# Optimization experiments

Measured on AMD Instinct MI355X. Metric: run time of the kernel, lower is better.

The kernel has to match this reference:

```python
import jax, jax.numpy as jnp
import numpy as np

B, L, H, D, M = 4, 2048, 16, 64, 128
EPS = 1e-6


def _create_projection_matrix(key, m, d):
    nb_full_blocks = m // d
    keys = jax.random.split(key, nb_full_blocks + 2)
    blocks = []
    for i in range(nb_full_blocks):
        unstructured = jax.random.normal(keys[i], (d, d), dtype=jnp.float32)
        q, _ = jnp.linalg.qr(unstructured)
        blocks.append(q.T)
    remaining = m - nb_full_blocks * d
    if remaining > 0:
        unstructured = jax.random.normal(keys[nb_full_blocks], (d, d), dtype=jnp.float32)
        q, _ = jnp.linalg.qr(unstructured)
        blocks.append(q.T[:remaining])
    final = jnp.concatenate(blocks, axis=0)  # [m, d]
    multiplier = jnp.linalg.norm(jax.random.normal(keys[-1], (m, d), dtype=jnp.float32), axis=1)
    return multiplier[:, None] * final


def setup_inputs() -> dict:
    key = jax.random.key(0)
    kq, kk, kv, kp = jax.random.split(key, 4)
    return {
        "q": jax.random.normal(kq, (B, L, H, D), dtype=jnp.float32),
        "k": jax.random.normal(kk, (B, L, H, D), dtype=jnp.float32),
        "v": jax.random.normal(kv, (B, L, H, D), dtype=jnp.float32),
        "projection_matrix": _create_projection_matrix(kp, M, D),
    }


def _softmax_kernel(data, proj, is_query, eps=EPS):
    # data: [B,L,H,D], proj: [M,D]
    data = (data.shape[-1] ** -0.25) * data
    ratio = proj.shape[0] ** -0.5
    data_dash = jnp.einsum('blhd,md->blhm', data, proj)  # [B,L,H,M]
    diag = jnp.sum(data * data, axis=-1, keepdims=True) * 0.5  # [B,L,H,1]
    if is_query:
        mx = jnp.max(data_dash, axis=-1, keepdims=True)
    else:
        mx = jnp.max(data_dash, axis=(1, 3), keepdims=True)
    return ratio * (jnp.exp(data_dash - diag - mx) + eps)


def reference(q, k, v, projection_matrix):
    qp = _softmax_kernel(q, projection_matrix, True)   # [B,L,H,M]
    kp = _softmax_kernel(k, projection_matrix, False)  # [B,L,H,M]
    # move L to the front for the causal scan
    qs = jnp.swapaxes(qp, 0, 1)  # [L,B,H,M]
    ks = jnp.swapaxes(kp, 0, 1)  # [L,B,H,M]
    vs = jnp.swapaxes(v, 0, 1)   # [L,B,H,D]

    def step(carry, inp):
        s, dsum = carry                 # s: [B,H,M,D], dsum: [B,H,M]
        q_t, k_t, v_t = inp
        s = s + k_t[..., :, None] * v_t[..., None, :]  # outer product accumulate
        dsum = dsum + k_t
        num = jnp.einsum('bhmd,bhm->bhd', s, q_t)      # [B,H,D]
        den = jnp.einsum('bhm,bhm->bh', q_t, dsum)     # [B,H]
        return (s, dsum), (num, den)

    init = (jnp.zeros((qs.shape[1], qs.shape[2], qs.shape[3], vs.shape[3]), qs.dtype),
            jnp.zeros_like(ks[0]))
    _, (nums, dens) = jax.lax.scan(step, init, (qs, ks, vs))
    av = jnp.swapaxes(nums, 0, 1)          # [B,L,H,D]
    norm = jnp.swapaxes(dens, 0, 1)[..., None]  # [B,L,H,1]
    return av / norm
```

## Files before the change

### kernel.cpp

```cpp
#include <hip/hip_runtime.h>
#include <math.h>

#define B_ 4
#define L_ 2048
#define H_ 16
#define D_ 64
#define M_ 128
#define TC_ 64
#define NC_ (L_ / TC_)
#define EPSK 1e-6f
#define DATA_SCALE 0.35355339059327379f
#define RATIO 0.08838834764831845f

typedef __bf16 bf16;
typedef bf16 bf16x4 __attribute__((ext_vector_type(4)));
typedef bf16 bf16x8 __attribute__((ext_vector_type(8)));
typedef float floatx4 __attribute__((ext_vector_type(4)));

#define PK64 72
#define FS_ 136

__device__ __forceinline__ unsigned pk(bf16 a, bf16 b) {
    return (unsigned)__builtin_bit_cast(unsigned short, a) |
           ((unsigned)__builtin_bit_cast(unsigned short, b) << 16);
}

__device__ __forceinline__ unsigned enc_f(float f) {
    unsigned u = __float_as_uint(f);
    return (u & 0x80000000u) ? ~u : (u | 0x80000000u);
}
__device__ __forceinline__ float dec_f(unsigned u) {
    unsigned b = (u & 0x80000000u) ? (u ^ 0x80000000u) : ~u;
    return __uint_as_float(b);
}

__global__ __launch_bounds__(256) void proj_split(const float* __restrict__ proj,
                                                  bf16* __restrict__ pfh,
                                                  bf16* __restrict__ pfl,
                                                  unsigned* __restrict__ mx) {
    int f = blockIdx.x * 256 + threadIdx.x;
    if (blockIdx.x == 0 && threadIdx.x < B_ * H_) mx[threadIdx.x] = 0u;
    int tc = f >> 7, k0h = (f >> 6) & 1, lane = f & 63;
    int lr = lane & 15, quad = lane >> 4;
    const float* src = proj + (16 * tc + lr) * 64 + k0h * 32 + quad * 8;
    float4 x0 = *(const float4*)src;
    float4 x1 = *(const float4*)(src + 4);
    float a[8] = {x0.x, x0.y, x0.z, x0.w, x1.x, x1.y, x1.z, x1.w};
    bf16x8 hi, lo;
#pragma unroll
    for (int e = 0; e < 8; e++) {
        bf16 h = (bf16)a[e];
        hi[e] = h;
        lo[e] = (bf16)(a[e] - (float)h);
    }
    *(bf16x8*)(pfh + (size_t)f * 8) = hi;
    *(bf16x8*)(pfl + (size_t)f * 8) = lo;
}

__global__ __launch_bounds__(256) void feat_max(const float* __restrict__ k,
                                                const bf16* __restrict__ pfh,
                                                unsigned* __restrict__ mxk) {
    __shared__ float wred[4];
    int tid = threadIdx.x;
    int blk = blockIdx.x;
    int c = blk & 31, h = (blk >> 5) & 15, b = blk >> 9;
    int l0 = c * 64;
    int w = tid >> 6, lane = tid & 63, lr = lane & 15, quad = lane >> 4;

    const float* drow = k +
        ((size_t)(b * L_ + l0 + 16 * w + lr) * H_ + h) * D_ + quad * 8;
    bf16x8 ah[2];
#pragma unroll
    for (int k0 = 0; k0 < 2; k0++) {
        float4 x0 = *(const float4*)(drow + k0 * 32);
        float4 x1 = *(const float4*)(drow + k0 * 32 + 4);
        float a[8] = {x0.x, x0.y, x0.z, x0.w, x1.x, x1.y, x1.z, x1.w};
#pragma unroll
        for (int e = 0; e < 8; e++) ah[k0][e] = (bf16)(DATA_SCALE * a[e]);
    }

    floatx4 acc[8];
#pragma unroll
    for (int tc = 0; tc < 8; tc++) acc[tc] = (floatx4){0.f, 0.f, 0.f, 0.f};
    const bf16x8* ph = (const bf16x8*)pfh + lane;
#pragma unroll
    for (int tc = 0; tc < 8; tc++)
#pragma unroll
        for (int k0 = 0; k0 < 2; k0++) {
            bf16x8 bh = ph[(tc * 2 + k0) * 64];
            acc[tc] = __builtin_amdgcn_mfma_f32_16x16x32_bf16(ah[k0], bh, acc[tc], 0, 0, 0);
        }

    float mm = acc[0][0];
#pragma unroll
    for (int tc = 0; tc < 8; tc++)
#pragma unroll
        for (int reg = 0; reg < 4; reg++) mm = fmaxf(mm, acc[tc][reg]);
#pragma unroll
    for (int off = 1; off < 64; off <<= 1) mm = fmaxf(mm, __shfl_xor(mm, off, 64));
    if (lane == 0) wred[w] = mm;
    __syncthreads();
    if (tid == 0) {
        float g = fmaxf(fmaxf(wred[0], wred[1]), fmaxf(wred[2], wred[3]));
        atomicMax(&mxk[b * H_ + h], enc_f(g));
    }
}

__global__ __launch_bounds__(256) void feat_k(const float* __restrict__ kin,
                                              const bf16* __restrict__ pfh,
                                              const bf16* __restrict__ pfl,
                                              const unsigned* __restrict__ mxk,
                                              bf16* __restrict__ kp) {
    __shared__ __align__(16) bf16 sc[64 * 130];
    int tid = threadIdx.x;
    int blk = blockIdx.x;
    int c = blk & 31, h = (blk >> 5) & 15, b = blk >> 9;
    int l0 = c * 64;
    int w = tid >> 6, lane = tid & 63, lr = lane & 15, quad = lane >> 4;

    const float* drow = kin +
        ((size_t)(b * L_ + l0 + 16 * w + lr) * H_ + h) * D_ + quad * 8;
    bf16x8 ah[2], al[2];
    float ss = 0.f;
#pragma unroll
    for (int k0 = 0; k0 < 2; k0++) {
        float4 x0 = *(const float4*)(drow + k0 * 32);
        float4 x1 = *(const float4*)(drow + k0 * 32 + 4);
        float a[8] = {x0.x, x0.y, x0.z, x0.w, x1.x, x1.y, x1.z, x1.w};
#pragma unroll
        for (int e = 0; e < 8; e++) {
            float s = DATA_SCALE * a[e];
            ss += s * s;
            bf16 hh = (bf16)s;
            ah[k0][e] = hh;
            al[k0][e] = (bf16)(s - (float)hh);
        }
    }
    ss += __shfl_xor(ss, 16, 64);
    ss += __shfl_xor(ss, 32, 64);
    float ssrow = 0.5f * ss;

    floatx4 acc[8];
#pragma unroll
    for (int tc = 0; tc < 8; tc++) acc[tc] = (floatx4){0.f, 0.f, 0.f, 0.f};
    const bf16x8* ph = (const bf16x8*)pfh + lane;
    const bf16x8* pl = (const bf16x8*)pfl + lane;
#pragma unroll
    for (int tc = 0; tc < 8; tc++)
#pragma unroll
        for (int k0 = 0; k0 < 2; k0++) {
            bf16x8 bh = ph[(tc * 2 + k0) * 64];
            bf16x8 bl = pl[(tc * 2 + k0) * 64];
            acc[tc] = __builtin_amdgcn_mfma_f32_16x16x32_bf16(ah[k0], bh, acc[tc], 0, 0, 0);
            acc[tc] = __builtin_amdgcn_mfma_f32_16x16x32_bf16(al[k0], bh, acc[tc], 0, 0, 0);
            acc[tc] = __builtin_amdgcn_mfma_f32_16x16x32_bf16(ah[k0], bl, acc[tc], 0, 0, 0);
        }

    int t0 = 16 * w + 4 * quad;
    float mxg = dec_f(mxk[b * H_ + h]);
#pragma unroll
    for (int reg = 0; reg < 4; reg++) {
        float dg = __shfl(ssrow, 4 * quad + reg, 64);
        float sh = dg + mxg;
#pragma unroll
        for (int tc = 0; tc < 8; tc++) {
            float val = RATIO * (__expf(acc[tc][reg] - sh) + EPSK);
            sc[(t0 + reg) * 130 + 16 * tc + lr] = (bf16)val;
        }
    }
    __syncthreads();

    unsigned* kout = (unsigned*)(kp + (size_t)blk * 8192);
#pragma unroll
    for (int i = 0; i < 16; i++) {
        int u = tid + 256 * i;
        int f = u >> 2, e0 = (u & 3) * 2;
        int fi = f >> 6, fl = f & 63;
        int tau = 16 * (fi & 3) + (fl & 15);
        int m = 32 * (fi >> 2) + 8 * (fl >> 4) + e0;
        kout[u] = pk(sc[tau * 130 + m], sc[tau * 130 + m + 1]);
    }
}

__global__ __launch_bounds__(256) void chunk_v(const bf16* __restrict__ kp,
                                               const float* __restrict__ v,
                                               bf16* __restrict__ S,
                                               float* __restrict__ ds,
                                               bf16* __restrict__ vbT) {
    __shared__ __align__(16) bf16 kT[128 * PK64];
    __shared__ __align__(16) bf16 vT[64 * PK64];
    int tid = threadIdx.x;
    int blk = blockIdx.x;
    int c = blk & 31, bh = blk >> 5;
    int h = bh & 15, b = bh >> 4;
    int l0 = c * 64;
    int w = tid >> 6, lane = tid & 63, lr = lane & 15, quad = lane >> 4;

    const bf16* kpt = kp + (size_t)blk * 8192;
#pragma unroll
    for (int i = 0; i < 4; i++) {
        int m8 = w * 4 + i;
        bf16x8 kv = *(const bf16x8*)(kpt +
            (((m8 >> 2) * 4 + (lane >> 4)) * 64 + (m8 & 3) * 16 + (lane & 15)) * 8);
#pragma unroll
        for (int e = 0; e < 8; e++) kT[(m8 * 8 + e) * PK64 + lane] = kv[e];
    }
    {
        const float* vrow = v + ((size_t)(b * L_ + l0 + lane) * H_ + h) * D_;
#pragma unroll
        for (int i = 0; i < 4; i++) {
            int d4 = w * 4 + i;
            float4 x = *(const float4*)(vrow + d4 * 4);
            vT[(d4 * 4 + 0) * PK64 + lane] = (bf16)x.x;
            vT[(d4 * 4 + 1) * PK64 + lane] = (bf16)x.y;
            vT[(d4 * 4 + 2) * PK64 + lane] = (bf16)x.z;
            vT[(d4 * 4 + 3) * PK64 + lane] = (bf16)x.w;
        }
    }
    __syncthreads();

    floatx4 acc[8];
#pragma unroll
    for (int tc = 0; tc < 8; tc++) acc[tc] = (floatx4){0.f, 0.f, 0.f, 0.f};
#pragma unroll
    for (int k0 = 0; k0 < 64; k0 += 32) {
        bf16x8 a = *(const bf16x8*)(vT + (16 * w + lr) * PK64 + k0 + quad * 8);
#pragma unroll
        for (int tc = 0; tc < 8; tc++) {
            bf16x8 bb = *(const bf16x8*)(kT + (16 * tc + lr) * PK64 + k0 + quad * 8);
            acc[tc] = __builtin_amdgcn_mfma_f32_16x16x32_bf16(a, bb, acc[tc], 0, 0, 0);
        }
    }

    {
        size_t ob = (size_t)(bh * D_) * (size_t)L_ + l0;
#pragma unroll
        for (int i = 0; i < 8; i++) {
            int e2 = tid + 256 * i;
            int d = e2 >> 5, tau2 = (e2 & 31) * 2;
            *(unsigned*)(vbT + ob + (size_t)d * L_ + tau2) =
                *(const unsigned*)(vT + d * PK64 + tau2);
        }
    }

    float dsv = 0.f;
    {
        int m = tid >> 1, half = tid & 1;
        const bf16x8* kr = (const bf16x8*)(kT + m * PK64 + half * 32);
#pragma unroll
        for (int j = 0; j < 4; j++) {
            bf16x8 vv = kr[j];
#pragma unroll
            for (int e = 0; e < 8; e++) dsv += (float)vv[e];
        }
        dsv += __shfl_xor(dsv, 1, 64);
    }
    __syncthreads();

    bf16* scr = kT;
#pragma unroll
    for (int tc = 0; tc < 8; tc++)
#pragma unroll
        for (int reg = 0; reg < 4; reg++)
            scr[((tc >> 1) * 4 + w) * 512 +
                (((((tc & 1) << 1) | (lr >> 3)) * 16) + 4 * quad + reg) * 8 +
                (lr & 7)] = (bf16)acc[tc][reg];
    if ((tid & 1) == 0) ds[(size_t)blk * M_ + (tid >> 1)] = dsv;
    __syncthreads();
#pragma unroll
    for (int i = 0; i < 4; i++) {
        int e = tid + 256 * i;
        ((uint4*)S)[(size_t)blk * 1024 + e] = ((const uint4*)scr)[e];
    }
}

__global__ void prefix_SD(unsigned* __restrict__ S, float* __restrict__ ds) {
    int blk = blockIdx.x;
    int seg = blk & 15, bh = blk >> 4;
    int p = seg * 256 + threadIdx.x;
    size_t base = (size_t)bh * NC_ * 4096 + p;
    unsigned uv[NC_];
#pragma unroll
    for (int c = 0; c < NC_; c++) uv[c] = S[base + (size_t)c * 4096];
    float c0 = 0.f, c1 = 0.f;
#pragma unroll
    for (int c = 0; c < NC_; c++) {
        unsigned u = uv[c];
        float f0 = (float)__builtin_bit_cast(bf16, (unsigned short)(u & 0xffffu));
        float f1 = (float)__builtin_bit_cast(bf16, (unsigned short)(u >> 16));
        S[base + (size_t)c * 4096] = pk((bf16)c0, (bf16)c1);
        c0 += f0; c1 += f1;
    }
    if (seg == 0 && threadIdx.x < 128) {
        int m = threadIdx.x;
        size_t dbase = (size_t)bh * NC_ * M_ + m;
        float dv[NC_];
#pragma unroll
        for (int c = 0; c < NC_; c++) dv[c] = ds[dbase + (size_t)c * M_];
        float carry = 0.f;
#pragma unroll
        for (int c = 0; c < NC_; c++) {
            ds[dbase + (size_t)c * M_] = carry;
            carry += dv[c];
        }
    }
}

__global__ __launch_bounds__(256, 3) void attn_q(const float* __restrict__ q,
                                                 const bf16* __restrict__ pfh,
                                                 const bf16* __restrict__ pfl,
                                                 const bf16* __restrict__ kp,
                                                 const bf16* __restrict__ vbT,
                                                 const bf16* __restrict__ Sp,
                                                 const float* __restrict__ dp,
                                                 float* __restrict__ out) {
    __shared__ __align__(16) bf16 fsc[64 * FS_];
    __shared__ __align__(16) bf16 vT[64 * PK64];
    __shared__ float dprevL[128];

    int tid = threadIdx.x;
    int blk = blockIdx.x;
    int c = blk & 31, bh = blk >> 5;
    int h = bh & 15, b = bh >> 4;
    int l0 = c * 64;
    int w = tid >> 6, lane = tid & 63, lr = lane & 15, quad = lane >> 4;

    bf16x8 spf[16];
    {
        const bf16x8* spb = (const bf16x8*)(Sp + (size_t)blk * 8192) + lane;
#pragma unroll
        for (int f = 0; f < 16; f++) spf[f] = spb[f * 64];
    }
#pragma unroll
    for (int i = 0; i < 2; i++) {
        int ch = tid + 256 * i;
        int d = ch >> 3, c8 = ch & 7;
        *(uint4*)(vT + d * PK64 + c8 * 8) =
            ((const uint4*)vbT)[(((size_t)bh * D_ + d) * L_ + l0) / 8 + c8];
    }
    if (tid < 128) dprevL[tid] = dp[(size_t)blk * M_ + tid];

    const float* drow = q +
        ((size_t)(b * L_ + l0 + 16 * w + lr) * H_ + h) * D_ + quad * 8;
    bf16x8 ah[2], al[2];
    float ss = 0.f;
#pragma unroll
    for (int k0 = 0; k0 < 2; k0++) {
        float4 x0 = *(const float4*)(drow + k0 * 32);
        float4 x1 = *(const float4*)(drow + k0 * 32 + 4);
        float a[8] = {x0.x, x0.y, x0.z, x0.w, x1.x, x1.y, x1.z, x1.w};
#pragma unroll
        for (int e = 0; e < 8; e++) {
            float s = DATA_SCALE * a[e];
            ss += s * s;
            bf16 hh = (bf16)s;
            ah[k0][e] = hh;
            al[k0][e] = (bf16)(s - (float)hh);
        }
    }
    ss += __shfl_xor(ss, 16, 64);
    ss += __shfl_xor(ss, 32, 64);
    float ssrow = 0.5f * ss;

    floatx4 facc[8];
#pragma unroll
    for (int tc = 0; tc < 8; tc++) facc[tc] = (floatx4){0.f, 0.f, 0.f, 0.f};
    {
        const bf16x8* ph = (const bf16x8*)pfh + lane;
        const bf16x8* pl = (const bf16x8*)pfl + lane;
#pragma unroll
        for (int tc = 0; tc < 8; tc++)
#pragma unroll
            for (int k0 = 0; k0 < 2; k0++) {
                bf16x8 bh = ph[(tc * 2 + k0) * 64];
                bf16x8 bl = pl[(tc * 2 + k0) * 64];
                facc[tc] = __builtin_amdgcn_mfma_f32_16x16x32_bf16(ah[k0], bh, facc[tc], 0, 0, 0);
                facc[tc] = __builtin_amdgcn_mfma_f32_16x16x32_bf16(al[k0], bh, facc[tc], 0, 0, 0);
                facc[tc] = __builtin_amdgcn_mfma_f32_16x16x32_bf16(ah[k0], bl, facc[tc], 0, 0, 0);
            }
    }
    int t0 = 16 * w + 4 * quad;
#pragma unroll
    for (int reg = 0; reg < 4; reg++) {
        float m = facc[0][reg];
#pragma unroll
        for (int tc = 1; tc < 8; tc++) m = fmaxf(m, facc[tc][reg]);
        m = fmaxf(m, __shfl_xor(m, 1, 64));
        m = fmaxf(m, __shfl_xor(m, 2, 64));
        m = fmaxf(m, __shfl_xor(m, 4, 64));
        m = fmaxf(m, __shfl_xor(m, 8, 64));
        float dg = __shfl(ssrow, 4 * quad + reg, 64);
        float sh = dg + m;
#pragma unroll
        for (int tc = 0; tc < 8; tc++) {
            float val = RATIO * (__expf(facc[tc][reg] - sh) + EPSK);
            fsc[(t0 + reg) * FS_ + 16 * tc + lr] = (bf16)val;
        }
    }

    bf16x8 af[4];
#pragma unroll
    for (int k = 0; k < 4; k++)
        af[k] = *(const bf16x8*)(fsc + (16 * w + lr) * FS_ + 32 * k + quad * 8);

    floatx4 acc[4];
#pragma unroll
    for (int tc = 0; tc < 4; tc++) acc[tc] = (floatx4){0.f, 0.f, 0.f, 0.f};

#pragma unroll
    for (int ki = 0; ki < 4; ki++)
#pragma unroll
        for (int tc = 0; tc < 4; tc++)
            acc[tc] = __builtin_amdgcn_mfma_f32_16x16x32_bf16(af[ki], spf[ki * 4 + tc],
                                                              acc[tc], 0, 0, 0);

    floatx4 acc2[4];
#pragma unroll
    for (int tc = 0; tc < 4; tc++) acc2[tc] = (floatx4){0.f, 0.f, 0.f, 0.f};
    {
        const bf16x8* kpb = (const bf16x8*)(kp + (size_t)blk * 8192) + lane;
        bf16x8 kb[16];
#pragma unroll
        for (int f = 0; f < 16; f++) kb[f] = kpb[f * 64];
#pragma unroll
        for (int ki = 0; ki < 4; ki++)
#pragma unroll
            for (int tc = 0; tc < 4; tc++)
                if (tc <= w)
                    acc2[tc] = __builtin_amdgcn_mfma_f32_16x16x32_bf16(af[ki], kb[ki * 4 + tc],
                                                                       acc2[tc], 0, 0, 0);
    }

    float densc[4];
    {
        float dsum[4] = {0.f, 0.f, 0.f, 0.f};
#pragma unroll
        for (int tc = 0; tc < 4; tc++) {
#pragma unroll
            for (int reg = 0; reg < 4; reg++) {
                int tg = t0 + reg, tau = 16 * tc + lr;
                float vv = (tc <= w) ? acc2[tc][reg] : 0.f;
                if (tau > tg) vv = 0.f;
                dsum[reg] += vv;
                fsc[tg * FS_ + tau] = (bf16)vv;
            }
        }
#pragma unroll
        for (int reg = 0; reg < 4; reg++) {
            float s = dsum[reg];
            s += __shfl_xor(s, 1, 64);
            s += __shfl_xor(s, 2, 64);
            s += __shfl_xor(s, 4, 64);
            s += __shfl_xor(s, 8, 64);
            densc[reg] = s;
        }
    }

    __syncthreads();

    float den0v = 0.f;
#pragma unroll
    for (int k = 0; k < 4; k++)
#pragma unroll
        for (int e = 0; e < 8; e++)
            den0v += (float)af[k][e] * dprevL[quad * 8 + 32 * k + e];
    den0v += __shfl_xor(den0v, 16, 64);
    den0v += __shfl_xor(den0v, 32, 64);

    {
        int kmax = (w >= 2) ? 64 : 32;
        for (int k0 = 0; k0 < kmax; k0 += 32) {
            bf16x8 a = *(const bf16x8*)(fsc + (16 * w + lr) * FS_ + k0 + quad * 8);
#pragma unroll
            for (int tc = 0; tc < 4; tc++) {
                bf16x8 bb = *(const bf16x8*)(vT + (16 * tc + lr) * PK64 + k0 + quad * 8);
                acc[tc] = __builtin_amdgcn_mfma_f32_16x16x32_bf16(a, bb, acc[tc], 0, 0, 0);
            }
        }
    }

    {
        float inv[4];
#pragma unroll
        for (int reg = 0; reg < 4; reg++) {
            float d0 = __shfl(den0v, 4 * quad + reg, 64);
            inv[reg] = 1.0f / (d0 + densc[reg]);
        }
#pragma unroll
        for (int tc = 0; tc < 4; tc++)
#pragma unroll
            for (int reg = 0; reg < 4; reg++)
                out[((size_t)(b * L_ + l0 + t0 + reg) * H_ + h) * D_ + 16 * tc + lr] =
                    acc[tc][reg] * inv[reg];
    }
}

extern "C" void kernel_launch(void* const* d_in, const int* in_sizes, int n_in,
                              void* d_out, int out_size, void* d_ws, size_t ws_size,
                              hipStream_t stream) {
    const float* q = (const float*)d_in[0];
    const float* k = (const float*)d_in[1];
    const float* v = (const float*)d_in[2];
    const float* proj = (const float*)d_in[3];
    float* out = (float*)d_out;
    char* W = (char*)d_ws;

    bf16* kp   = (bf16*)(W);
    bf16* vbT  = (bf16*)(W + 33554432ull);
    bf16* S    = (bf16*)(W + 50331648ull);
    float* ds  = (float*)(W + 83886080ull);
    unsigned* mx = (unsigned*)(W + 84934656ull);
    bf16* pfh  = (bf16*)(W + 84934912ull);
    bf16* pfl  = (bf16*)(W + 84951296ull);

    hipLaunchKernelGGL(proj_split, dim3(4), dim3(256), 0, stream, proj, pfh, pfl, mx);
    hipLaunchKernelGGL(feat_max, dim3(2048), dim3(256), 0, stream, k, pfh, mx);
    hipLaunchKernelGGL(feat_k, dim3(2048), dim3(256), 0, stream, k, pfh, pfl, mx, kp);
    hipLaunchKernelGGL(chunk_v, dim3(2048), dim3(256), 0, stream, kp, v, S, ds, vbT);
    hipLaunchKernelGGL(prefix_SD, dim3(1024), dim3(256), 0, stream, (unsigned*)S, ds);
    hipLaunchKernelGGL(attn_q, dim3(2048), dim3(256), 0, stream,
                       q, pfh, pfl, kp, vbT, S, ds, out);
}
```

Baseline: 231.8 us.

## Drop LDS staging and barriers in attn_q, raise occupancy, vectorize feat_k stores

In attn_q, the V-transpose and previous-denominator vectors are now read straight from global memory instead of being staged in shared memory. The S-prefix fragments are loaded just before their MFMA use rather than at kernel start, and the __syncthreads calls are removed. Together these cut LDS use and live registers so launch bounds can ask for 4 blocks per CU instead of 3. In feat_k, each wave writes its own rows back from shared memory with 16-byte stores and no block barrier, replacing the scattered 32-bit packed stores. The cost is more uncached-looking global loads from each wave, and the code relies on each wave reading only the shared-memory rows it wrote itself.

```diff
diff --git a/kernel.cpp b/kernel.cpp
--- a/kernel.cpp
+++ b/kernel.cpp
@@ -111,7 +111,7 @@
                                               const bf16* __restrict__ pfl,
                                               const unsigned* __restrict__ mxk,
                                               bf16* __restrict__ kp) {
-    __shared__ __align__(16) bf16 sc[64 * 130];
+    __shared__ __align__(16) bf16 sc[64 * FS_];
     int tid = threadIdx.x;
     int blk = blockIdx.x;
     int c = blk & 31, h = (blk >> 5) & 15, b = blk >> 9;
@@ -165,20 +165,16 @@
 #pragma unroll
         for (int tc = 0; tc < 8; tc++) {
             float val = RATIO * (__expf(acc[tc][reg] - sh) + EPSK);
-            sc[(t0 + reg) * 130 + 16 * tc + lr] = (bf16)val;
-        }
-    }
-    __syncthreads();
-
-    unsigned* kout = (unsigned*)(kp + (size_t)blk * 8192);
-#pragma unroll
-    for (int i = 0; i < 16; i++) {
-        int u = tid + 256 * i;
-        int f = u >> 2, e0 = (u & 3) * 2;
-        int fi = f >> 6, fl = f & 63;
-        int tau = 16 * (fi & 3) + (fl & 15);
-        int m = 32 * (fi >> 2) + 8 * (fl >> 4) + e0;
-        kout[u] = pk(sc[tau * 130 + m], sc[tau * 130 + m + 1]);
+            sc[(t0 + reg) * FS_ + 16 * tc + lr] = (bf16)val;
+        }
+    }
+
+    {
+        uint4* kout = (uint4*)(kp + (size_t)blk * 8192);
+#pragma unroll
+        for (int ki = 0; ki < 4; ki++)
+            kout[(ki * 4 + w) * 64 + lane] =
+                *(const uint4*)(sc + (16 * w + lr) * FS_ + 32 * ki + 8 * quad);
     }
 }
 
@@ -306,7 +302,7 @@
     }
 }
 
-__global__ __launch_bounds__(256, 3) void attn_q(const float* __restrict__ q,
+__global__ __launch_bounds__(256, 4) void attn_q(const float* __restrict__ q,
                                                  const bf16* __restrict__ pfh,
                                                  const bf16* __restrict__ pfl,
                                                  const bf16* __restrict__ kp,
@@ -315,8 +311,6 @@
                                                  const float* __restrict__ dp,
                                                  float* __restrict__ out) {
     __shared__ __align__(16) bf16 fsc[64 * FS_];
-    __shared__ __align__(16) bf16 vT[64 * PK64];
-    __shared__ float dprevL[128];
 
     int tid = threadIdx.x;
     int blk = blockIdx.x;
@@ -324,21 +318,6 @@
     int h = bh & 15, b = bh >> 4;
     int l0 = c * 64;
     int w = tid >> 6, lane = tid & 63, lr = lane & 15, quad = lane >> 4;
-
-    bf16x8 spf[16];
-    {
-        const bf16x8* spb = (const bf16x8*)(Sp + (size_t)blk * 8192) + lane;
-#pragma unroll
-        for (int f = 0; f < 16; f++) spf[f] = spb[f * 64];
-    }
-#pragma unroll
-    for (int i = 0; i < 2; i++) {
-        int ch = tid + 256 * i;
-        int d = ch >> 3, c8 = ch & 7;
-        *(uint4*)(vT + d * PK64 + c8 * 8) =
-            ((const uint4*)vbT)[(((size_t)bh * D_ + d) * L_ + l0) / 8 + c8];
-    }
-    if (tid < 128) dprevL[tid] = dp[(size_t)blk * M_ + tid];
 
     const float* drow = q +
         ((size_t)(b * L_ + l0 + 16 * w + lr) * H_ + h) * D_ + quad * 8;
@@ -407,12 +386,18 @@
 #pragma unroll
     for (int tc = 0; tc < 4; tc++) acc[tc] = (floatx4){0.f, 0.f, 0.f, 0.f};
 
-#pragma unroll
-    for (int ki = 0; ki < 4; ki++)
-#pragma unroll
-        for (int tc = 0; tc < 4; tc++)
-            acc[tc] = __builtin_amdgcn_mfma_f32_16x16x32_bf16(af[ki], spf[ki * 4 + tc],
-                                                              acc[tc], 0, 0, 0);
+    {
+        const bf16x8* spb = (const bf16x8*)(Sp + (size_t)blk * 8192) + lane;
+        bf16x8 sp4[16];
+#pragma unroll
+        for (int f = 0; f < 16; f++) sp4[f] = spb[f * 64];
+#pragma unroll
+        for (int ki = 0; ki < 4; ki++)
+#pragma unroll
+            for (int tc = 0; tc < 4; tc++)
+                acc[tc] = __builtin_amdgcn_mfma_f32_16x16x32_bf16(af[ki], sp4[ki * 4 + tc],
+                                                                  acc[tc], 0, 0, 0);
+    }
 
     floatx4 acc2[4];
 #pragma unroll
@@ -456,24 +441,30 @@
         }
     }
 
-    __syncthreads();
-
     float den0v = 0.f;
-#pragma unroll
-    for (int k = 0; k < 4; k++)
-#pragma unroll
-        for (int e = 0; e < 8; e++)
-            den0v += (float)af[k][e] * dprevL[quad * 8 + 32 * k + e];
+    {
+        const float* dpb = dp + (size_t)blk * M_ + quad * 8;
+#pragma unroll
+        for (int k = 0; k < 4; k++) {
+            float4 d0 = *(const float4*)(dpb + 32 * k);
+            float4 d1 = *(const float4*)(dpb + 32 * k + 4);
+            den0v += (float)af[k][0] * d0.x + (float)af[k][1] * d0.y +
+                     (float)af[k][2] * d0.z + (float)af[k][3] * d0.w +
+                     (float)af[k][4] * d1.x + (float)af[k][5] * d1.y +
+                     (float)af[k][6] * d1.z + (float)af[k][7] * d1.w;
+        }
+    }
     den0v += __shfl_xor(den0v, 16, 64);
     den0v += __shfl_xor(den0v, 32, 64);
 
     {
+        const bf16* vbb = vbT + (size_t)(bh * D_) * L_ + l0 + quad * 8;
         int kmax = (w >= 2) ? 64 : 32;
         for (int k0 = 0; k0 < kmax; k0 += 32) {
             bf16x8 a = *(const bf16x8*)(fsc + (16 * w + lr) * FS_ + k0 + quad * 8);
 #pragma unroll
             for (int tc = 0; tc < 4; tc++) {
-                bf16x8 bb = *(const bf16x8*)(vT + (16 * tc + lr) * PK64 + k0 + quad * 8);
+                bf16x8 bb = *(const bf16x8*)(vbb + (size_t)(16 * tc + lr) * L_ + k0);
                 acc[tc] = __builtin_amdgcn_mfma_f32_16x16x32_bf16(a, bb, acc[tc], 0, 0, 0);
             }
         }
```

Result: faster. 223.7 us (-3.5%).
